# Kernel optimization log

Hardware: AMD Instinct MI355X
Metric: run time of the kernel (lower is better)

## Reference

```python
import jax, jax.numpy as jnp
import numpy as np

B, L, D, K = 16, 1024, 1024, 3
EPS_LN = 1e-5    # nn.LayerNorm default eps inside SRUCell
EPS_RMS = 1e-6   # RMSNorm eps
HIGHWAY_BIAS = -2.0


def setup_inputs() -> dict:
    key = jax.random.key(0)
    ks = jax.random.split(key, 8)
    x = jax.random.normal(ks[0], (B, L, D), jnp.float32)
    conv_w = jax.random.normal(ks[1], (D, D, K), jnp.float32) * (1.0 / np.sqrt(D * K))
    conv_b = jax.random.normal(ks[2], (D,), jnp.float32) * 0.01
    ln_g = jnp.ones((D,), jnp.float32)
    ln_b = jnp.zeros((D,), jnp.float32)
    sru_w = jax.random.normal(ks[3], (D, 3 * D), jnp.float32) * (1.0 / np.sqrt(D))
    sru_v = jax.random.uniform(ks[4], (2 * D,), jnp.float32, -0.18, 0.18)
    # SRU init: forget-gate bias 0, reset-gate bias = highway_bias
    sru_b = jnp.concatenate([jnp.zeros((D,), jnp.float32),
                             jnp.full((D,), HIGHWAY_BIAS, jnp.float32)])
    lambda_w = jax.random.normal(ks[5], (D,), jnp.float32)
    rms_w = jnp.ones((D,), jnp.float32)
    return {"x": x, "conv_w": conv_w, "conv_b": conv_b, "ln_g": ln_g,
            "ln_b": ln_b, "sru_w": sru_w, "sru_v": sru_v, "sru_b": sru_b,
            "lambda_w": lambda_w, "rms_w": rms_w}


def reference(x, conv_w, conv_b, ln_g, ln_b, sru_w, sru_v, sru_b, lambda_w, rms_w):
    # --- causal conv1d: left-pad K-1 zeros, 'VALID' conv -> same length ---
    xT = jnp.transpose(x, (0, 2, 1))                      # (B, D, L)
    xp = jnp.pad(xT, ((0, 0), (0, 0), (K - 1, 0)))
    y = jax.lax.conv_general_dilated(
        xp, conv_w, window_strides=(1,), padding='VALID',
        dimension_numbers=('NCH', 'OIH', 'NCH')) + conv_b[None, :, None]
    cnn_out = jnp.transpose(y, (2, 0, 1))                 # (L, B, D) time-major

    # --- SRUCell with layer_norm=True: LN on input, then U = x @ W (k=3) ---
    mu = jnp.mean(cnn_out, -1, keepdims=True)
    var = jnp.mean((cnn_out - mu) ** 2, -1, keepdims=True)
    normed = (cnn_out - mu) * jax.lax.rsqrt(var + EPS_LN) * ln_g + ln_b
    U = jnp.einsum('lbd,de->lbe', normed, sru_w).reshape(L, B, D, 3)

    v_f, v_r = sru_v[:D], sru_v[D:]
    b_f, b_r = sru_b[:D], sru_b[D:]

    def step(c, inputs):
        u, xt = inputs                                    # u: (B, D, 3), xt: (B, D)
        u0, u1, u2 = u[..., 0], u[..., 1], u[..., 2]
        f = jax.nn.sigmoid(u1 + v_f * c + b_f)
        c_new = f * c + (1.0 - f) * u0
        r = jax.nn.sigmoid(u2 + v_r * c + b_r)
        h = r * jnp.tanh(c_new) + (1.0 - r) * xt          # highway (scale_x = 1)
        return c_new, h

    c0 = jnp.zeros((B, D), jnp.float32)
    _, h = jax.lax.scan(step, c0, (U, normed))            # h: (L, B, D)

    # --- lambda-weighted residual mix ---
    out = lambda_w * cnn_out + (1.0 - lambda_w) * h       # (L, B, D)
    out = jnp.transpose(out, (1, 0, 2))                   # (B, L, D)

    # --- RMSNorm (dropout is identity in eval) ---
    rms = out * jax.lax.rsqrt(jnp.mean(out * out, -1, keepdims=True) + EPS_RMS)
    return rms_w * rms
```

## Files before the change

kernel.cpp:

```cpp
#include <hip/hip_runtime.h>
#include <cstdint>
#include <cstddef>

#define LL 1024
#define DD 1024
#define BB 16

typedef _Float16 f16;
typedef _Float16 f16x8 __attribute__((ext_vector_type(8)));
typedef _Float16 f16x4 __attribute__((ext_vector_type(4)));
typedef float f32x4 __attribute__((ext_vector_type(4)));

__global__ __launch_bounds__(256) void xsplit_kernel(const float* __restrict__ x,
                                                     f16* __restrict__ xh) {
    int i = blockIdx.x * 256 + threadIdx.x;
    const int total = BB * LL * DD / 4;
    if (i >= total) return;
    float4 v = ((const float4*)x)[i];
    f16x4 h;
    h[0] = (f16)v.x; h[1] = (f16)v.y; h[2] = (f16)v.z; h[3] = (f16)v.w;
    ((f16x4*)xh)[i] = h;
}

__global__ __launch_bounds__(256) void wkt_kernel(const float* __restrict__ w,
                                                  f16* __restrict__ wkT) {
    int idx = blockIdx.x * 256 + threadIdx.x;
    if (idx >= 3 * DD * DD) return;
    int o = idx / 3072;
    int r = idx - o * 3072;
    int k = r >> 10, i = r & 1023;
    wkT[idx] = (f16)w[(size_t)o * 3072 + i * 3 + k];
}

__global__ __launch_bounds__(256) void swt_kernel(const float* __restrict__ w,
                                                  f16* __restrict__ swT) {
    int idx = blockIdx.x * 256 + threadIdx.x;
    if (idx >= 3 * DD * DD) return;
    int e = idx >> 10, d = idx & 1023;
    swT[idx] = (f16)w[(size_t)d * 3072 + e];
}

__global__ __launch_bounds__(128) void zp_kernel(f16* __restrict__ zp) {
    zp[threadIdx.x] = (f16)0;
}

__global__ __launch_bounds__(256) void hgemm_kernel(
    const f16* __restrict__ A, const f16* __restrict__ BT,
    const float* __restrict__ bias, float* __restrict__ C,
    const f16* __restrict__ zp,
    int N, int Kdim, int mode, int l0, int tpb, int Lc) {
    __shared__ f16 sm[2][2][128 * 64];
    const int tid = threadIdx.x;
    const int lane = tid & 63, wave = tid >> 6;
    const int wm = wave & 1, wn = wave >> 1;
    const int n0 = blockIdx.x * 128;

    int arowbase, crowbase;
    if (mode == 0) {
        arowbase = blockIdx.y * 128;
        crowbase = arowbase;
    } else {
        int bb = blockIdx.y / tpb, lt = blockIdx.y - bb * tpb;
        arowbase = (bb << 10) + l0 + lt * 128;
        crowbase = bb * Lc + lt * 128;
    }

    auto stageA = [&](int kt, int buf) {
#pragma unroll
        for (int i = 0; i < 4; ++i) {
            int row = wave * 32 + i * 8 + (lane >> 3);
            int chunk = (lane & 7) ^ (row & 7);
            const f16* src;
            if (mode == 0) {
                int m = arowbase + row;
                int bb2 = m >> 10, l = m & 1023;
                int kc = kt >> 10;
                int t = l + kc - 2;
                src = (t < 0) ? (zp + chunk * 8)
                              : (A + (((size_t)(bb2 << 10) + t) << 10) +
                                 (kt & 1023) + chunk * 8);
            } else {
                src = A + ((size_t)(arowbase + row) << 10) + kt + chunk * 8;
            }
            __builtin_amdgcn_global_load_lds(
                (const __attribute__((address_space(1))) void*)src,
                (__attribute__((address_space(3))) void*)&sm[buf][0][(wave * 32 + i * 8) * 64],
                16, 0, 0);
        }
    };
    auto stageB = [&](int kt, int buf) {
#pragma unroll
        for (int i = 0; i < 4; ++i) {
            int row = wave * 32 + i * 8 + (lane >> 3);
            int chunk = (lane & 7) ^ (row & 7);
            const f16* src = BT + (size_t)(n0 + row) * Kdim + kt + chunk * 8;
            __builtin_amdgcn_global_load_lds(
                (const __attribute__((address_space(1))) void*)src,
                (__attribute__((address_space(3))) void*)&sm[buf][1][(wave * 32 + i * 8) * 64],
                16, 0, 0);
        }
    };

    f32x4 acc[4][4];
#pragma unroll
    for (int i = 0; i < 4; ++i)
#pragma unroll
        for (int j = 0; j < 4; ++j)
#pragma unroll
            for (int r = 0; r < 4; ++r) acc[i][j][r] = 0.f;

    stageA(0, 0);
    stageB(0, 0);
    asm volatile("s_waitcnt vmcnt(0)" ::: "memory");
    __syncthreads();

    const int kbyte = (lane >> 4) * 16;
    const int rA = wm * 64 + (lane & 15);
    const int rB = wn * 64 + (lane & 15);

    int cur = 0;
    for (int kt = 0; kt < Kdim; kt += 64) {
        if (kt + 64 < Kdim) {
            stageA(kt + 64, cur ^ 1);
            stageB(kt + 64, cur ^ 1);
        }
        const char* Ap = (const char*)&sm[cur][0][0];
        const char* Bp = (const char*)&sm[cur][1][0];
#pragma unroll
        for (int ks = 0; ks < 2; ++ks) {
            f16x8 a[4], b[4];
#pragma unroll
            for (int f = 0; f < 4; ++f) {
                int rowa = rA + f * 16;
                a[f] = *(const f16x8*)(Ap + rowa * 128 +
                                       ((ks * 64 + kbyte) ^ ((rowa & 7) << 4)));
                int rowb = rB + f * 16;
                b[f] = *(const f16x8*)(Bp + rowb * 128 +
                                       ((ks * 64 + kbyte) ^ ((rowb & 7) << 4)));
            }
#pragma unroll
            for (int fi = 0; fi < 4; ++fi)
#pragma unroll
                for (int fj = 0; fj < 4; ++fj)
                    acc[fi][fj] = __builtin_amdgcn_mfma_f32_16x16x32_f16(
                        a[fi], b[fj], acc[fi][fj], 0, 0, 0);
        }
        asm volatile("s_waitcnt vmcnt(0)" ::: "memory");
        __syncthreads();
        cur ^= 1;
    }

    float bv[4];
#pragma unroll
    for (int fj = 0; fj < 4; ++fj)
        bv[fj] = bias ? bias[n0 + wn * 64 + fj * 16 + (lane & 15)] : 0.f;
#pragma unroll
    for (int fi = 0; fi < 4; ++fi) {
        int row0 = crowbase + wm * 64 + fi * 16 + ((lane >> 4) << 2);
#pragma unroll
        for (int fj = 0; fj < 4; ++fj) {
            int col = n0 + wn * 64 + fj * 16 + (lane & 15);
            float* cp = C + (size_t)row0 * N + col;
#pragma unroll
            for (int r = 0; r < 4; ++r)
                cp[(size_t)r * N] = acc[fi][fj][r] + bv[fj];
        }
    }
}

__global__ __launch_bounds__(256) void ln_kernel(const float* __restrict__ in,
                                                 const float* __restrict__ g,
                                                 const float* __restrict__ be,
                                                 float* __restrict__ outp,
                                                 f16* __restrict__ outh) {
    const int m = blockIdx.x;
    const int t = threadIdx.x;
    const float4 v = ((const float4*)(in + ((size_t)m << 10)))[t];
    float s = v.x + v.y + v.z + v.w;
    float q = v.x * v.x + v.y * v.y + v.z * v.z + v.w * v.w;
#pragma unroll
    for (int off = 32; off; off >>= 1) {
        s += __shfl_down(s, off);
        q += __shfl_down(q, off);
    }
    __shared__ float red[8];
    const int wv = t >> 6, ln = t & 63;
    if (ln == 0) { red[wv] = s; red[4 + wv] = q; }
    __syncthreads();
    float S = red[0] + red[1] + red[2] + red[3];
    float Q = red[4] + red[5] + red[6] + red[7];
    float mu  = S * (1.f / 1024.f);
    float var = Q * (1.f / 1024.f) - mu * mu;
    float inv = rsqrtf(var + 1e-5f);
    float4 g4  = ((const float4*)g)[t];
    float4 b4  = ((const float4*)be)[t];
    float4 o;
    o.x = (v.x - mu) * inv * g4.x + b4.x;
    o.y = (v.y - mu) * inv * g4.y + b4.y;
    o.z = (v.z - mu) * inv * g4.z + b4.z;
    o.w = (v.w - mu) * inv * g4.w + b4.w;
    ((float4*)(outp + ((size_t)m << 10)))[t] = o;
    f16x4 h;
    h[0] = (f16)o.x; h[1] = (f16)o.y; h[2] = (f16)o.z; h[3] = (f16)o.w;
    ((f16x4*)(outh + ((size_t)m << 10)))[t] = h;
}

__device__ __forceinline__ float sigmoid_f(float x) {
    return __builtin_amdgcn_rcpf(1.f + __expf(-x));
}
__device__ __forceinline__ float tanh_f(float x) {
    float e = __expf(2.f * x);
    return 1.f - 2.f * __builtin_amdgcn_rcpf(e + 1.f);
}

__global__ __launch_bounds__(64) void scan_kernel(const float* __restrict__ U,
                                                  const float* __restrict__ nrm,
                                                  const float* __restrict__ cnn,
                                                  const float* __restrict__ v_in,
                                                  const float* __restrict__ b_in,
                                                  const float* __restrict__ lam,
                                                  float* __restrict__ outp,
                                                  float* __restrict__ c_state,
                                                  int l0, int Lc) {
    const int tid = blockIdx.x * 64 + threadIdx.x;
    const int b = tid >> 10, d = tid & 1023;
    const float vf = v_in[d], vr = v_in[DD + d];
    const float bf = b_in[d], br = b_in[DD + d];
    const float lw = lam[d];
    const float* Up = U + (size_t)b * Lc * 3072 + 3 * d;
    const size_t rowbase = (((size_t)(b << 10) + l0) << 10) + d;
    const float* xp = nrm + rowbase;
    const float* cp = cnn + rowbase;
    float*       op = outp + rowbase;

    float c = (l0 == 0) ? 0.f : c_state[tid];
    constexpr int CH = 8;
    float A0[CH], A1[CH], A2[CH], AX[CH], AC[CH];
    float B0[CH], B1[CH], B2[CH], BX[CH], BC[CH];

#pragma unroll
    for (int j = 0; j < CH; ++j) {
        size_t lu = (size_t)j * 3072, lx = (size_t)j << 10;
        A0[j] = Up[lu]; A1[j] = Up[lu + 1]; A2[j] = Up[lu + 2];
        AX[j] = xp[lx]; AC[j] = cp[lx];
    }

    for (int ll0 = 0; ll0 < Lc; ll0 += 2 * CH) {
#pragma unroll
        for (int j = 0; j < CH; ++j) {
            int ll = ll0 + CH + j;
            size_t lu = (size_t)ll * 3072, lx = (size_t)ll << 10;
            B0[j] = Up[lu]; B1[j] = Up[lu + 1]; B2[j] = Up[lu + 2];
            BX[j] = xp[lx]; BC[j] = cp[lx];
        }
#pragma unroll
        for (int j = 0; j < CH; ++j) {
            float f = sigmoid_f(A1[j] + vf * c + bf);
            float r = sigmoid_f(A2[j] + vr * c + br);
            float cn = fmaf(f, c - A0[j], A0[j]);
            float h  = r * tanh_f(cn) + (1.f - r) * AX[j];
            c = cn;
            op[(size_t)(ll0 + j) << 10] = fmaf(lw, AC[j] - h, h);
        }
        if (ll0 + 2 * CH < Lc) {
#pragma unroll
            for (int j = 0; j < CH; ++j) {
                int ll = ll0 + 2 * CH + j;
                size_t lu = (size_t)ll * 3072, lx = (size_t)ll << 10;
                A0[j] = Up[lu]; A1[j] = Up[lu + 1]; A2[j] = Up[lu + 2];
                AX[j] = xp[lx]; AC[j] = cp[lx];
            }
        }
#pragma unroll
        for (int j = 0; j < CH; ++j) {
            float f = sigmoid_f(B1[j] + vf * c + bf);
            float r = sigmoid_f(B2[j] + vr * c + br);
            float cn = fmaf(f, c - B0[j], B0[j]);
            float h  = r * tanh_f(cn) + (1.f - r) * BX[j];
            c = cn;
            op[(size_t)(ll0 + CH + j) << 10] = fmaf(lw, BC[j] - h, h);
        }
    }
    c_state[tid] = c;
}

__global__ __launch_bounds__(256) void rms_kernel(float* __restrict__ io,
                                                  const float* __restrict__ w) {
    const int m = blockIdx.x;
    const int t = threadIdx.x;
    float4 v = ((float4*)(io + ((size_t)m << 10)))[t];
    float q = v.x * v.x + v.y * v.y + v.z * v.z + v.w * v.w;
#pragma unroll
    for (int off = 32; off; off >>= 1) q += __shfl_down(q, off);
    __shared__ float red[4];
    const int wv = t >> 6, ln = t & 63;
    if (ln == 0) red[wv] = q;
    __syncthreads();
    float Q = red[0] + red[1] + red[2] + red[3];
    float inv = rsqrtf(Q * (1.f / 1024.f) + 1e-6f);
    float4 w4 = ((const float4*)w)[t];
    v.x *= inv * w4.x;
    v.y *= inv * w4.y;
    v.z *= inv * w4.z;
    v.w *= inv * w4.w;
    ((float4*)(io + ((size_t)m << 10)))[t] = v;
}

extern "C" void kernel_launch(void* const* d_in, const int* in_sizes, int n_in,
                              void* d_out, int out_size, void* d_ws, size_t ws_size,
                              hipStream_t stream) {
    const float* x        = (const float*)d_in[0];
    const float* conv_w   = (const float*)d_in[1];
    const float* conv_b   = (const float*)d_in[2];
    const float* ln_g     = (const float*)d_in[3];
    const float* ln_b     = (const float*)d_in[4];
    const float* sru_w    = (const float*)d_in[5];
    const float* sru_v    = (const float*)d_in[6];
    const float* sru_b    = (const float*)d_in[7];
    const float* lambda_w = (const float*)d_in[8];
    const float* rms_w    = (const float*)d_in[9];
    float* out = (float*)d_out;

    f16* x_h   = (f16*)d_ws;
    f16* nrm_h = x_h   + (size_t)16 * 1024 * 1024;
    f16* wkT   = nrm_h + (size_t)16 * 1024 * 1024;
    f16* swT   = wkT   + (size_t)3 * 1024 * 1024;
    f16* zp    = swT   + (size_t)3 * 1024 * 1024;
    float* cnn     = (float*)(zp + 1024);
    float* c_state = cnn + (size_t)16 * 1024 * 1024;
    float* U_buf   = c_state + 16384;

    const size_t fixed_bytes = ((size_t)38 * 1024 * 1024 + 1024) * 2
                             + ((size_t)16 * 1024 * 1024 + 16384) * 4;
    int Lc = 128;
    for (int cand = 1024; cand >= 128; cand >>= 1) {
        if (fixed_bytes + (size_t)16 * cand * 3072 * 4 <= ws_size) { Lc = cand; break; }
    }
    const int tpb = Lc / 128;
    float* nrm = out;

    xsplit_kernel<<<dim3(16384), dim3(256), 0, stream>>>(x, x_h);
    wkt_kernel<<<dim3(12288), dim3(256), 0, stream>>>(conv_w, wkT);
    swt_kernel<<<dim3(12288), dim3(256), 0, stream>>>(sru_w, swT);
    zp_kernel<<<dim3(1), dim3(128), 0, stream>>>(zp);
    hgemm_kernel<<<dim3(8, 128), dim3(256), 0, stream>>>(x_h, wkT, conv_b, cnn,
                                                         zp, 1024, 3072, 0, 0, 0, 0);
    ln_kernel<<<dim3(16384), dim3(256), 0, stream>>>(cnn, ln_g, ln_b, nrm, nrm_h);
    for (int l0 = 0; l0 < LL; l0 += Lc) {
        hgemm_kernel<<<dim3(24, 16 * tpb), dim3(256), 0, stream>>>(
            nrm_h, swT, nullptr, U_buf, zp, 3072, 1024, 1, l0, tpb, Lc);
        scan_kernel<<<dim3(256), dim3(64), 0, stream>>>(
            U_buf, nrm, cnn, sru_v, sru_b, lambda_w, out, c_state, l0, Lc);
    }
    rms_kernel<<<dim3(16384), dim3(256), 0, stream>>>(out, rms_w);
}
```

Before: 599.6 us.

## Store U and normed input in fp16, tile weight transposes, template GEMM with grouped grid

The U projection is now written as fp16, and the scan reads the fp16 normed input instead of a separate fp32 copy. This halves U traffic, removes the fp32 normed write in LN, and may let a larger chunk Lc fit in the workspace. The weight transpose kernels now go through shared memory so their global accesses coalesce. The GEMM is templated on mode and sizes and uses a 1D grid remapped into groups of 8 row tiles for L2 reuse. The cost is extra fp16 rounding on U and on the highway input term.

```diff
diff --git a/kernel.cpp b/kernel.cpp
--- a/kernel.cpp
+++ b/kernel.cpp
@@ -24,43 +24,68 @@
 
 __global__ __launch_bounds__(256) void wkt_kernel(const float* __restrict__ w,
                                                   f16* __restrict__ wkT) {
-    int idx = blockIdx.x * 256 + threadIdx.x;
-    if (idx >= 3 * DD * DD) return;
-    int o = idx / 3072;
-    int r = idx - o * 3072;
-    int k = r >> 10, i = r & 1023;
-    wkT[idx] = (f16)w[(size_t)o * 3072 + i * 3 + k];
+    __shared__ float s[3072];
+    const int o = blockIdx.x;
+    const int t = threadIdx.x;
+    const float* src = w + (size_t)o * 3072;
+#pragma unroll
+    for (int rep = 0; rep < 12; ++rep) s[rep * 256 + t] = src[rep * 256 + t];
+    __syncthreads();
+    f16* dst = wkT + (size_t)o * 3072;
+#pragma unroll
+    for (int rep = 0; rep < 12; ++rep) {
+        int j = rep * 256 + t;
+        int k = j >> 10, i = j & 1023;
+        dst[j] = (f16)s[i * 3 + k];
+    }
 }
 
 __global__ __launch_bounds__(256) void swt_kernel(const float* __restrict__ w,
                                                   f16* __restrict__ swT) {
-    int idx = blockIdx.x * 256 + threadIdx.x;
-    if (idx >= 3 * DD * DD) return;
-    int e = idx >> 10, d = idx & 1023;
-    swT[idx] = (f16)w[(size_t)d * 3072 + e];
+    __shared__ float s[64][65];
+    const int et = blockIdx.x, dt = blockIdx.y;
+    const int t = threadIdx.x;
+    const int tr = t >> 6, tc = t & 63;
+#pragma unroll
+    for (int i = 0; i < 16; ++i) {
+        int d = dt * 64 + i * 4 + tr;
+        s[i * 4 + tr][tc] = w[(size_t)d * 3072 + et * 64 + tc];
+    }
+    __syncthreads();
+#pragma unroll
+    for (int i = 0; i < 16; ++i) {
+        int e = i * 4 + tr;
+        swT[(size_t)(et * 64 + e) * 1024 + dt * 64 + tc] = (f16)s[tc][e];
+    }
 }
 
 __global__ __launch_bounds__(128) void zp_kernel(f16* __restrict__ zp) {
     zp[threadIdx.x] = (f16)0;
 }
 
+template <int MODE, int NN, int KK, bool OUTF16>
 __global__ __launch_bounds__(256) void hgemm_kernel(
     const f16* __restrict__ A, const f16* __restrict__ BT,
-    const float* __restrict__ bias, float* __restrict__ C,
-    const f16* __restrict__ zp,
-    int N, int Kdim, int mode, int l0, int tpb, int Lc) {
+    const float* __restrict__ bias, void* __restrict__ Cv,
+    const f16* __restrict__ zp, int l0, int tpb, int Lc) {
     __shared__ f16 sm[2][2][128 * 64];
     const int tid = threadIdx.x;
     const int lane = tid & 63, wave = tid >> 6;
     const int wm = wave & 1, wn = wave >> 1;
-    const int n0 = blockIdx.x * 128;
+    constexpr int nx = NN / 128;
+
+    const int id = blockIdx.x;
+    const int r8 = id & 7, s = id >> 3;
+    const int bx = s % nx;
+    const int by = (s / nx) * 8 + r8;
+    const int n0 = bx * 128;
 
     int arowbase, crowbase;
-    if (mode == 0) {
-        arowbase = blockIdx.y * 128;
+    if (MODE == 0) {
+        arowbase = by * 128;
         crowbase = arowbase;
     } else {
-        int bb = blockIdx.y / tpb, lt = blockIdx.y - bb * tpb;
+        int bb = by / tpb, lt = by - bb * tpb;
         arowbase = (bb << 10) + l0 + lt * 128;
         crowbase = bb * Lc + lt * 128;
     }
@@ -71,7 +96,7 @@
             int row = wave * 32 + i * 8 + (lane >> 3);
             int chunk = (lane & 7) ^ (row & 7);
             const f16* src;
-            if (mode == 0) {
+            if (MODE == 0) {
                 int m = arowbase + row;
                 int bb2 = m >> 10, l = m & 1023;
                 int kc = kt >> 10;
@@ -93,7 +118,7 @@
         for (int i = 0; i < 4; ++i) {
             int row = wave * 32 + i * 8 + (lane >> 3);
             int chunk = (lane & 7) ^ (row & 7);
-            const f16* src = BT + (size_t)(n0 + row) * Kdim + kt + chunk * 8;
+            const f16* src = BT + (size_t)(n0 + row) * KK + kt + chunk * 8;
             __builtin_amdgcn_global_load_lds(
                 (const __attribute__((address_space(1))) void*)src,
                 (__attribute__((address_space(3))) void*)&sm[buf][1][(wave * 32 + i * 8) * 64],
@@ -119,8 +144,8 @@
     const int rB = wn * 64 + (lane & 15);
 
     int cur = 0;
-    for (int kt = 0; kt < Kdim; kt += 64) {
-        if (kt + 64 < Kdim) {
+    for (int kt = 0; kt < KK; kt += 64) {
+        if (kt + 64 < KK) {
             stageA(kt + 64, cur ^ 1);
             stageB(kt + 64, cur ^ 1);
         }
@@ -153,17 +178,24 @@
     float bv[4];
 #pragma unroll
     for (int fj = 0; fj < 4; ++fj)
-        bv[fj] = bias ? bias[n0 + wn * 64 + fj * 16 + (lane & 15)] : 0.f;
+        bv[fj] = (!OUTF16 && bias) ? bias[n0 + wn * 64 + fj * 16 + (lane & 15)] : 0.f;
 #pragma unroll
     for (int fi = 0; fi < 4; ++fi) {
         int row0 = crowbase + wm * 64 + fi * 16 + ((lane >> 4) << 2);
 #pragma unroll
         for (int fj = 0; fj < 4; ++fj) {
             int col = n0 + wn * 64 + fj * 16 + (lane & 15);
-            float* cp = C + (size_t)row0 * N + col;
-#pragma unroll
-            for (int r = 0; r < 4; ++r)
-                cp[(size_t)r * N] = acc[fi][fj][r] + bv[fj];
+            if (OUTF16) {
+                f16* cp = (f16*)Cv + (size_t)row0 * NN + col;
+#pragma unroll
+                for (int r = 0; r < 4; ++r)
+                    cp[(size_t)r * NN] = (f16)acc[fi][fj][r];
+            } else {
+                float* cp = (float*)Cv + (size_t)row0 * NN + col;
+#pragma unroll
+                for (int r = 0; r < 4; ++r)
+                    cp[(size_t)r * NN] = acc[fi][fj][r] + bv[fj];
+            }
         }
     }
 }
@@ -171,7 +203,6 @@
 __global__ __launch_bounds__(256) void ln_kernel(const float* __restrict__ in,
                                                  const float* __restrict__ g,
                                                  const float* __restrict__ be,
-                                                 float* __restrict__ outp,
                                                  f16* __restrict__ outh) {
     const int m = blockIdx.x;
     const int t = threadIdx.x;
@@ -194,14 +225,11 @@
     float inv = rsqrtf(var + 1e-5f);
     float4 g4  = ((const float4*)g)[t];
     float4 b4  = ((const float4*)be)[t];
-    float4 o;
-    o.x = (v.x - mu) * inv * g4.x + b4.x;
-    o.y = (v.y - mu) * inv * g4.y + b4.y;
-    o.z = (v.z - mu) * inv * g4.z + b4.z;
-    o.w = (v.w - mu) * inv * g4.w + b4.w;
-    ((float4*)(outp + ((size_t)m << 10)))[t] = o;
     f16x4 h;
-    h[0] = (f16)o.x; h[1] = (f16)o.y; h[2] = (f16)o.z; h[3] = (f16)o.w;
+    h[0] = (f16)((v.x - mu) * inv * g4.x + b4.x);
+    h[1] = (f16)((v.y - mu) * inv * g4.y + b4.y);
+    h[2] = (f16)((v.z - mu) * inv * g4.z + b4.z);
+    h[3] = (f16)((v.w - mu) * inv * g4.w + b4.w);
     ((f16x4*)(outh + ((size_t)m << 10)))[t] = h;
 }
 
@@ -213,8 +241,8 @@
     return 1.f - 2.f * __builtin_amdgcn_rcpf(e + 1.f);
 }
 
-__global__ __launch_bounds__(64) void scan_kernel(const float* __restrict__ U,
-                                                  const float* __restrict__ nrm,
+__global__ __launch_bounds__(64) void scan_kernel(const f16* __restrict__ U,
+                                                  const f16* __restrict__ nrm_h,
                                                   const float* __restrict__ cnn,
                                                   const float* __restrict__ v_in,
                                                   const float* __restrict__ b_in,
@@ -227,9 +255,9 @@
     const float vf = v_in[d], vr = v_in[DD + d];
     const float bf = b_in[d], br = b_in[DD + d];
     const float lw = lam[d];
-    const float* Up = U + (size_t)b * Lc * 3072 + 3 * d;
+    const f16* Up = U + (size_t)b * Lc * 3072 + 3 * d;
     const size_t rowbase = (((size_t)(b << 10) + l0) << 10) + d;
-    const float* xp = nrm + rowbase;
+    const f16*   xp = nrm_h + rowbase;
     const float* cp = cnn + rowbase;
     float*       op = outp + rowbase;
 
@@ -241,8 +269,8 @@
 #pragma unroll
     for (int j = 0; j < CH; ++j) {
         size_t lu = (size_t)j * 3072, lx = (size_t)j << 10;
-        A0[j] = Up[lu]; A1[j] = Up[lu + 1]; A2[j] = Up[lu + 2];
-        AX[j] = xp[lx]; AC[j] = cp[lx];
+        A0[j] = (float)Up[lu]; A1[j] = (float)Up[lu + 1]; A2[j] = (float)Up[lu + 2];
+        AX[j] = (float)xp[lx]; AC[j] = cp[lx];
     }
 
     for (int ll0 = 0; ll0 < Lc; ll0 += 2 * CH) {
@@ -250,8 +278,8 @@
         for (int j = 0; j < CH; ++j) {
             int ll = ll0 + CH + j;
             size_t lu = (size_t)ll * 3072, lx = (size_t)ll << 10;
-            B0[j] = Up[lu]; B1[j] = Up[lu + 1]; B2[j] = Up[lu + 2];
-            BX[j] = xp[lx]; BC[j] = cp[lx];
+            B0[j] = (float)Up[lu]; B1[j] = (float)Up[lu + 1]; B2[j] = (float)Up[lu + 2];
+            BX[j] = (float)xp[lx]; BC[j] = cp[lx];
         }
 #pragma unroll
         for (int j = 0; j < CH; ++j) {
@@ -267,8 +295,8 @@
             for (int j = 0; j < CH; ++j) {
                 int ll = ll0 + 2 * CH + j;
                 size_t lu = (size_t)ll * 3072, lx = (size_t)ll << 10;
-                A0[j] = Up[lu]; A1[j] = Up[lu + 1]; A2[j] = Up[lu + 2];
-                AX[j] = xp[lx]; AC[j] = cp[lx];
+                A0[j] = (float)Up[lu]; A1[j] = (float)Up[lu + 1]; A2[j] = (float)Up[lu + 2];
+                AX[j] = (float)xp[lx]; AC[j] = cp[lx];
             }
         }
 #pragma unroll
@@ -321,36 +349,38 @@
     const float* rms_w    = (const float*)d_in[9];
     float* out = (float*)d_out;
 
+    const size_t fixed_f16 = (size_t)38 * 1024 * 1024 + 1024;
+    const size_t f32_bytes = ((size_t)16 * 1024 * 1024 + 16384) * 4;
+    int Lc = 128;
+    for (int cand = 1024; cand >= 128; cand >>= 1) {
+        if (fixed_f16 * 2 + (size_t)16 * cand * 3072 * 2 + f32_bytes <= ws_size) {
+            Lc = cand; break;
+        }
+    }
+    const int tpb = Lc / 128;
+
     f16* x_h   = (f16*)d_ws;
     f16* nrm_h = x_h   + (size_t)16 * 1024 * 1024;
     f16* wkT   = nrm_h + (size_t)16 * 1024 * 1024;
     f16* swT   = wkT   + (size_t)3 * 1024 * 1024;
     f16* zp    = swT   + (size_t)3 * 1024 * 1024;
-    float* cnn     = (float*)(zp + 1024);
+    f16* U_h   = zp + 1024;
+    float* cnn     = (float*)(U_h + (size_t)16 * Lc * 3072);
     float* c_state = cnn + (size_t)16 * 1024 * 1024;
-    float* U_buf   = c_state + 16384;
-
-    const size_t fixed_bytes = ((size_t)38 * 1024 * 1024 + 1024) * 2
-                             + ((size_t)16 * 1024 * 1024 + 16384) * 4;
-    int Lc = 128;
-    for (int cand = 1024; cand >= 128; cand >>= 1) {
-        if (fixed_bytes + (size_t)16 * cand * 3072 * 4 <= ws_size) { Lc = cand; break; }
-    }
-    const int tpb = Lc / 128;
-    float* nrm = out;
 
     xsplit_kernel<<<dim3(16384), dim3(256), 0, stream>>>(x, x_h);
-    wkt_kernel<<<dim3(12288), dim3(256), 0, stream>>>(conv_w, wkT);
-    swt_kernel<<<dim3(12288), dim3(256), 0, stream>>>(sru_w, swT);
+    wkt_kernel<<<dim3(1024), dim3(256), 0, stream>>>(conv_w, wkT);
+    swt_kernel<<<dim3(48, 16), dim3(256), 0, stream>>>(sru_w, swT);
     zp_kernel<<<dim3(1), dim3(128), 0, stream>>>(zp);
-    hgemm_kernel<<<dim3(8, 128), dim3(256), 0, stream>>>(x_h, wkT, conv_b, cnn,
-                                                         zp, 1024, 3072, 0, 0, 0, 0);
-    ln_kernel<<<dim3(16384), dim3(256), 0, stream>>>(cnn, ln_g, ln_b, nrm, nrm_h);
+    hgemm_kernel<0, 1024, 3072, false>
+        <<<dim3(8 * 128), dim3(256), 0, stream>>>(x_h, wkT, conv_b, cnn, zp, 0, 0, 0);
+    ln_kernel<<<dim3(16384), dim3(256), 0, stream>>>(cnn, ln_g, ln_b, nrm_h);
     for (int l0 = 0; l0 < LL; l0 += Lc) {
-        hgemm_kernel<<<dim3(24, 16 * tpb), dim3(256), 0, stream>>>(
-            nrm_h, swT, nullptr, U_buf, zp, 3072, 1024, 1, l0, tpb, Lc);
+        hgemm_kernel<1, 3072, 1024, true>
+            <<<dim3(24 * 16 * tpb), dim3(256), 0, stream>>>(
+                nrm_h, swT, nullptr, U_h, zp, l0, tpb, Lc);
         scan_kernel<<<dim3(256), dim3(64), 0, stream>>>(
-            U_buf, nrm, cnn, sru_v, sru_b, lambda_w, out, c_state, l0, Lc);
+            U_h, nrm_h, cnn, sru_v, sru_b, lambda_w, out, c_state, l0, Lc);
     }
     rms_kernel<<<dim3(16384), dim3(256), 0, stream>>>(out, rms_w);
 }
```

Measured after the change: 553.7 us. -7.7%, faster.
